# Performance work log

Measured on AMD Instinct MI355X. Metric: run time of the kernel, lower is better.

Reference implementation:

```python
import jax, jax.numpy as jnp
import numpy as np

HEADS = 8
BN_EPS = 1e-5

def _bn(x2d, g, b):
    # torch BatchNorm1d in training mode: biased batch stats
    mu = x2d.mean(0)
    var = x2d.var(0)
    return (x2d - mu) * jax.lax.rsqrt(var + BN_EPS) * g + b

def _window_indices(H):
    # exclusive-end box coordinates, in the exact order of the torch loop
    m = H // 2
    r0, r1, c0, c1 = [], [], [], []
    for i in range(1, m + 1):
        wins = [(m - i, m + i + 1, m - i, m + i + 1),  # full square
                (m - i, m + 1,     m - i, m + i + 1),  # top half
                (m,     m + i + 1, m - i, m + i + 1),  # bottom half
                (m - i, m + i + 1, m - i, m + 1),      # left half
                (m - i, m + i + 1, m,     m + i + 1)]  # right half
        for a, b, c, d in wins:
            r0.append(a); r1.append(b); c0.append(c); c1.append(d)
    r0 = np.array(r0); r1 = np.array(r1); c0 = np.array(c0); c1 = np.array(c1)
    counts = ((r1 - r0) * (c1 - c0)).astype(np.float32)
    return r0, r1, c0, c1, counts

def _box_sums(P, r0, r1, c0, c1):
    # P: padded 2D prefix sum [B, C, H+1, H+1]; returns [B, C, K]
    return P[:, :, r1, c1] - P[:, :, r0, c1] - P[:, :, r1, c0] + P[:, :, r0, c0]

def _integral(img):
    return jnp.pad(jnp.cumsum(jnp.cumsum(img, axis=2), axis=3), ((0, 0), (0, 0), (1, 0), (1, 0)))

def setup_inputs() -> dict:
    key = jax.random.key(0)
    ks = jax.random.split(key, 8)
    B, Cin, H = 64, 512, 31
    C = 512  # heads * base_dim
    x = jax.random.normal(ks[0], (B, Cin, H, H), dtype=jnp.float32)
    w_v = jax.random.normal(ks[1], (Cin, C), dtype=jnp.float32) * 0.02
    w_k = jax.random.normal(ks[2], (Cin, C), dtype=jnp.float32) * 0.02
    w_fc = jax.random.normal(ks[3], (Cin + C, 512), dtype=jnp.float32) * 0.02
    z = lambda n: jnp.zeros((n,), jnp.float32)
    o = lambda n: jnp.ones((n,), jnp.float32)
    return {"x": x,
            "w_v": w_v, "b_v": z(C), "g_vn": o(C), "b_vn": z(C),
            "w_k": w_k, "b_k": z(C), "g_kn": o(C), "b_kn": z(C),
            "w_fc": w_fc, "b_fc": z(512), "g_fcn": o(512), "b_fcn": z(512)}

def reference(x, w_v, b_v, g_vn, b_vn, w_k, b_k, g_kn, b_kn, w_fc, b_fc, g_fcn, b_fcn):
    B, Cin, H, W = x.shape
    N = H * W
    C = w_v.shape[1]
    d = C // HEADS
    m = H // 2
    xt = x.reshape(B, Cin, N).transpose(0, 2, 1)       # [B, N, Cin]
    x0 = xt[:, N // 2, :]                              # [B, Cin] center pixel feature
    flat = xt.reshape(B * N, Cin)
    v = jax.nn.relu(_bn(flat @ w_v + b_v, g_vn, b_vn))
    v = v.reshape(B, N, C).transpose(0, 2, 1).reshape(B, C, H, H)
    k = _bn(flat @ w_k + b_k, g_kn, b_kn).reshape(B, N, HEADS, d).transpose(0, 2, 1, 3)  # [B,h,N,d]
    q = k[:, :, N // 2, :]                             # [B, h, d]
    attn = jax.nn.softmax(jnp.einsum('bhd,bhnd->bhn', q, k) * (d ** -0.5), axis=-1)      # [B,h,N]
    attn_full = jnp.broadcast_to(attn[:, :, None, :], (B, HEADS, d, N)).reshape(B, C, H, H)
    xw = attn_full * v                                 # attn-weighted values [B,C,H,H]
    eps = 1e-16
    r0, r1, c0, c1, counts = _window_indices(H)
    Px = _integral(xw)
    Pa = _integral(attn_full)
    mx = _box_sums(Px, r0, r1, c0, c1) / counts        # window means of xw   [B,C,K]
    ma = _box_sums(Pa, r0, r1, c0, c1) / counts        # window means of attn [B,C,K]
    y_win = (mx / (ma + eps)).transpose(0, 2, 1)       # [B, K, C]
    y = jnp.concatenate([xw[:, :, m, m][:, None, :], y_win], axis=1)  # [B, n, C]
    # F.normalize(p=2, dim=2)
    y = y / jnp.maximum(jnp.linalg.norm(y, axis=2, keepdims=True), 1e-12)
    n = y.shape[1]
    yy = jnp.concatenate([jnp.broadcast_to(x0[:, None, :], (B, n, Cin)), y], axis=-1)
    out = jax.nn.relu(_bn(yy.reshape(B * n, Cin + C) @ w_fc + b_fc, g_fcn, b_fcn))
    return out.reshape(B, n, -1)
```

## Files before the change

kernel.cpp:

```cpp
#include <hip/hip_runtime.h>
#include <stdint.h>

#define DEV __device__ __forceinline__

typedef __bf16 bf16x8 __attribute__((ext_vector_type(8)));
typedef unsigned short u16x8 __attribute__((ext_vector_type(8)));
typedef float f32x4 __attribute__((ext_vector_type(4)));

#define NS 968
#define NMB0 484
#define NMB1 38
#define RCH 16
#define NCH0 ((NMB0 + RCH - 1) / RCH)

DEV uint16_t f2bf(float f) {
    union { float f; uint32_t u; } v; v.f = f;
    uint32_t r = v.u + 0x7fffu + ((v.u >> 16) & 1u);
    return (uint16_t)(r >> 16);
}
DEV float bf2f(uint16_t h) {
    union { uint32_t u; float f; } v; v.u = ((uint32_t)h) << 16;
    return v.f;
}
DEV float bflo(uint32_t w) { union { uint32_t u; float f; } v; v.u = w << 16; return v.f; }
DEV float bfhi(uint32_t w) { union { uint32_t u; float f; } v; v.u = w & 0xffff0000u; return v.f; }

#if __has_builtin(__builtin_amdgcn_cvt_pk_bf16_f32)
typedef __bf16 bf16x2 __attribute__((ext_vector_type(2)));
DEV uint32_t pk2bf(float lo, float hi) {
    bf16x2 r = __builtin_amdgcn_cvt_pk_bf16_f32(lo, hi);
    return __builtin_bit_cast(uint32_t, r);
}
#else
DEV uint32_t pk2bf(float lo, float hi) {
    return (uint32_t)f2bf(lo) | ((uint32_t)f2bf(hi) << 16);
}
#endif

#if __has_builtin(__builtin_amdgcn_global_load_lds)
DEV void async16(const uint16_t* g, uint16_t* l) {
    __builtin_amdgcn_global_load_lds(
        (const __attribute__((address_space(1))) uint32_t*)g,
        (__attribute__((address_space(3))) uint32_t*)l, 16, 0, 0);
}
#else
DEV void async16(const uint16_t* g, uint16_t* l) {
    *(u16x8*)l = *(const u16x8*)g;
}
#endif

__global__ void k_convert_x(const float* __restrict__ x, uint16_t* __restrict__ xbt) {
    __shared__ float tile[32][33];
    int b = blockIdx.z;
    int n0 = blockIdx.x * 32;
    int c0 = blockIdx.y * 32;
    int tx = threadIdx.x, ty = threadIdx.y;
    #pragma unroll
    for (int i = 0; i < 4; ++i) {
        int c = c0 + ty + 8 * i;
        int n = n0 + tx;
        float v = 0.f;
        if (n < 961) v = x[((size_t)b * 512 + c) * 961 + n];
        tile[ty + 8 * i][tx] = v;
    }
    __syncthreads();
    int idx = ty * 32 + tx;
    int c4 = (idx & 7) * 4;
    int nl = idx >> 3;
    int n = n0 + nl;
    if (n < NS) {
        ushort4 val;
        val.x = f2bf(tile[c4 + 0][nl]);
        val.y = f2bf(tile[c4 + 1][nl]);
        val.z = f2bf(tile[c4 + 2][nl]);
        val.w = f2bf(tile[c4 + 3][nl]);
        *(ushort4*)&xbt[((size_t)b * NS + n) * 512 + c0 + c4] = val;
    }
}

__global__ void k_convert_w(const float* __restrict__ wv, const float* __restrict__ wk,
                            const float* __restrict__ wfc,
                            uint16_t* __restrict__ wvkt, uint16_t* __restrict__ wfct) {
    int idx = blockIdx.x * 256 + threadIdx.x;
    if (idx < 524288) {
        int j = idx >> 9, k = idx & 511;
        float v = (j < 512) ? wv[(size_t)k * 512 + j] : wk[(size_t)k * 512 + (j - 512)];
        wvkt[idx] = f2bf(v);
    } else {
        int t = idx - 524288;
        int j = t >> 10, k = t & 1023;
        wfct[t] = f2bf(wfc[(size_t)k * 512 + j]);
    }
}

template<int K, int EPI>
__global__ __launch_bounds__(256, 4)
void k_gemm(const uint16_t* __restrict__ A, const uint16_t* __restrict__ Bt,
            uint16_t* __restrict__ out_v, uint16_t* __restrict__ out_k,
            float* __restrict__ out_f,
            float* __restrict__ part)
{
    __shared__ __align__(16) uint16_t sbuf[16384];
    __shared__ float sStat[512];
    uint16_t* sA0 = sbuf;
    uint16_t* sA1 = sbuf + 4096;
    uint16_t* sB0 = sbuf + 8192;
    uint16_t* sB1 = sbuf + 12288;

    const int tid = threadIdx.x;
    const int wave = tid >> 6, lane = tid & 63;
    const int quad = lane >> 4, l16 = lane & 15;
    int m0, j0, mbi = 0;
    if constexpr (EPI == 0) {
        int lin = blockIdx.x;
        int xcd = lin & 7, rest = lin >> 3;
        int jb = rest & 7, mhi = rest >> 3;
        int mb = mhi * 8 + xcd;
        if (mb >= NMB0) return;
        m0 = mb * 128; j0 = jb * 128; mbi = mb;
    } else {
        m0 = blockIdx.y * 128; j0 = blockIdx.x * 128; mbi = blockIdx.y;
    }
    const int wm = wave >> 1, wj = wave & 1;

    const f32x4 fzero = {0.f, 0.f, 0.f, 0.f};
    f32x4 acc[4][4];
    #pragma unroll
    for (int i = 0; i < 4; ++i)
        #pragma unroll
        for (int j = 0; j < 4; ++j) acc[i][j] = fzero;

    const int c0 = tid;
    const int mA0 = c0 >> 2, kq0 = c0 & 3;
    const int c1 = tid + 256;
    const int mA1 = c1 >> 2, kq1 = c1 & 3;

    const int KT = K / 64;
    for (int kt = 0; kt < KT; ++kt) {
        const uint16_t* Ak = A + (size_t)m0 * K + kt * 64;
        const uint16_t* Bk = Bt + (size_t)j0 * K + kt * 64;
        async16(Ak + (size_t)mA0 * K + kq0 * 8,      &sA0[c0 * 8]);
        async16(Ak + (size_t)mA1 * K + kq1 * 8,      &sA0[c1 * 8]);
        async16(Ak + (size_t)mA0 * K + 32 + kq0 * 8, &sA1[c0 * 8]);
        async16(Ak + (size_t)mA1 * K + 32 + kq1 * 8, &sA1[c1 * 8]);
        async16(Bk + (size_t)mA0 * K + kq0 * 8,      &sB0[c0 * 8]);
        async16(Bk + (size_t)mA1 * K + kq1 * 8,      &sB0[c1 * 8]);
        async16(Bk + (size_t)mA0 * K + 32 + kq0 * 8, &sB1[c0 * 8]);
        async16(Bk + (size_t)mA1 * K + 32 + kq1 * 8, &sB1[c1 * 8]);
        __syncthreads();
        #pragma unroll
        for (int p = 0; p < 2; ++p) {
            const uint16_t* pA = p ? sA1 : sA0;
            const uint16_t* pB = p ? sB1 : sB0;
            bf16x8 af[4], bfr[4];
            #pragma unroll
            for (int i = 0; i < 4; ++i) {
                int m = wm * 64 + i * 16 + l16;
                u16x8 r = *(const u16x8*)&pA[m * 32 + quad * 8];
                af[i] = __builtin_bit_cast(bf16x8, r);
            }
            #pragma unroll
            for (int j = 0; j < 4; ++j) {
                int jj = wj * 64 + j * 16 + l16;
                u16x8 r = *(const u16x8*)&pB[jj * 32 + quad * 8];
                bfr[j] = __builtin_bit_cast(bf16x8, r);
            }
            #pragma unroll
            for (int i = 0; i < 4; ++i)
                #pragma unroll
                for (int j = 0; j < 4; ++j)
                    acc[i][j] = __builtin_amdgcn_mfma_f32_16x16x32_bf16(af[i], bfr[j], acc[i][j], 0, 0, 0);
        }
        __syncthreads();
    }

    #pragma unroll
    for (int j = 0; j < 4; ++j) {
        const int col_local = wj * 64 + j * 16 + l16;
        float ls = 0.f, lq = 0.f;
        #pragma unroll
        for (int i = 0; i < 4; ++i) {
            #pragma unroll
            for (int reg = 0; reg < 4; ++reg) {
                const float val = acc[i][j][reg];
                ls += val; lq += val * val;
                if constexpr (EPI == 1) {
                    const int r = m0 + wm * 64 + i * 16 + quad * 4 + reg;
                    out_f[(size_t)r * 512 + (j0 + col_local)] = val;
                }
            }
        }
        ls += __shfl_xor(ls, 16); lq += __shfl_xor(lq, 16);
        ls += __shfl_xor(ls, 32); lq += __shfl_xor(lq, 32);
        if (quad == 0) {
            sStat[wm * 128 + col_local] = ls;
            sStat[256 + wm * 128 + col_local] = lq;
        }
    }
    __syncthreads();
    if (tid < 128) {
        float s = sStat[tid] + sStat[128 + tid];
        float q = sStat[256 + tid] + sStat[384 + tid];
        if constexpr (EPI == 0) {
            part[(size_t)mbi * 1024 + (j0 + tid)] = s;
            part[(size_t)NMB0 * 1024 + (size_t)mbi * 1024 + (j0 + tid)] = q;
        } else {
            part[(size_t)mbi * 512 + (j0 + tid)] = s;
            part[(size_t)NMB1 * 512 + (size_t)mbi * 512 + (j0 + tid)] = q;
        }
    }

    if constexpr (EPI == 0) {
        #pragma unroll
        for (int ch = 0; ch < 2; ++ch) {
            if (wj == ch) {
                #pragma unroll
                for (int j = 0; j < 4; ++j) {
                    const int c = j * 16 + l16;
                    #pragma unroll
                    for (int i = 0; i < 4; ++i) {
                        const int rloc = wm * 64 + i * 16 + quad * 4;
                        uint2 pp;
                        pp.x = pk2bf(acc[i][j][0], acc[i][j][1]);
                        pp.y = pk2bf(acc[i][j][2], acc[i][j][3]);
                        *(uint2*)&sbuf[c * 136 + rloc] = pp;
                    }
                }
            }
            __syncthreads();
            const int jg = j0 + ch * 64;
            uint16_t* const outp = (jg < 512) ? out_v : out_k;
            const int jbase = (jg < 512) ? jg : jg - 512;
            #pragma unroll
            for (int s = 0; s < 8; ++s) {
                const int chunk = tid + 256 * s;
                const int c = chunk >> 5, q = chunk & 31;
                uint2 val = *(const uint2*)&sbuf[c * 136 + q * 4];
                const int r = m0 + q * 4;
                const unsigned bb_ = (unsigned)r / (unsigned)NS;
                const unsigned nn = (unsigned)r - bb_ * (unsigned)NS;
                *(uint2*)&outp[((size_t)bb_ * 512 + jbase + c) * NS + nn] = val;
            }
            __syncthreads();
        }
    }
}

template<int NMB, int NC>
__global__ void k_redA(const float* __restrict__ part, float* __restrict__ pp)
{
    int col = blockIdx.x * 256 + threadIdx.x;
    int cz = blockIdx.y;
    int i0 = cz * RCH;
    float s = 0.f, q = 0.f;
    #pragma unroll
    for (int k = 0; k < RCH; ++k) {
        int i = i0 + k;
        if (i < NMB) {
            s += part[(size_t)i * NC + col];
            q += part[(size_t)(NMB + i) * NC + col];
        }
    }
    int nch = (NMB + RCH - 1) / RCH;
    pp[(size_t)cz * NC + col] = s;
    pp[(size_t)(nch + cz) * NC + col] = q;
}

template<int NCH, int NC>
__global__ void k_redB(const float* __restrict__ pp, float* __restrict__ osum,
                       float* __restrict__ osq)
{
    int col = blockIdx.x * 256 + threadIdx.x;
    float s = 0.f, q = 0.f;
    #pragma unroll
    for (int k = 0; k < NCH; ++k) {
        s += pp[(size_t)k * NC + col];
        q += pp[(size_t)(NCH + k) * NC + col];
    }
    osum[col] = s;
    osq[col] = q;
}

template<int NMB, int NC>
__global__ void k_redsmall(const float* __restrict__ part, float* __restrict__ osum,
                           float* __restrict__ osq)
{
    int col = blockIdx.x * 256 + threadIdx.x;
    float s = 0.f, q = 0.f;
    #pragma unroll
    for (int i = 0; i < NMB; ++i) {
        s += part[(size_t)i * NC + col];
        q += part[(size_t)(NMB + i) * NC + col];
    }
    osum[col] = s;
    osq[col] = q;
}

__global__ void k_attn(const uint16_t* __restrict__ kraw,
                       const float* __restrict__ colsum, const float* __restrict__ colsq,
                       const float* __restrict__ g_kn, const float* __restrict__ b_kn,
                       float* __restrict__ attn, float* __restrict__ maw)
{
    __shared__ float qa[64];
    __shared__ float s_qb;
    __shared__ float att[NS];
    __shared__ float red[8];

    int bh = blockIdx.x;
    int b = bh >> 3, h = bh & 7;
    int tid = threadIdx.x;
    constexpr float invM = 1.f / 61504.f;

    if (tid < 64) {
        int c = h * 64 + tid;
        float mean = colsum[512 + c] * invM;
        float q_ = colsq[512 + c] * invM;
        float a = g_kn[c] * rsqrtf(q_ - mean * mean + 1e-5f);
        float bb = b_kn[c] - mean * a;
        float kr = bf2f(kraw[((size_t)b * 512 + c) * NS + 480]);
        float qv = kr * a + bb;
        qa[tid] = qv * a;
        float qb = qv * bb;
        for (int off = 32; off; off >>= 1) qb += __shfl_down(qb, off);
        if (tid == 0) s_qb = qb;
    }
    __syncthreads();

    const int n4 = tid * 4;
    const bool active = n4 < 961;
    float a0 = 0.f, a1 = 0.f, a2 = 0.f, a3 = 0.f;
    if (active) {
        const uint16_t* kp = kraw + ((size_t)b * 512 + h * 64) * NS + n4;
        #pragma unroll 16
        for (int dd = 0; dd < 64; ++dd) {
            uint2 kk = *(const uint2*)(kp + (size_t)dd * NS);
            float q = qa[dd];
            a0 += q * bflo(kk.x);
            a1 += q * bfhi(kk.x);
            a2 += q * bflo(kk.y);
            a3 += q * bfhi(kk.y);
        }
    }
    float lg[4] = {a0, a1, a2, a3};
    float lmax = -1e30f;
    #pragma unroll
    for (int i = 0; i < 4; ++i) {
        lg[i] = (lg[i] + s_qb) * 0.125f;
        if (n4 + i < 961) lmax = fmaxf(lmax, lg[i]);
    }
    for (int off = 32; off; off >>= 1) lmax = fmaxf(lmax, __shfl_xor(lmax, off));
    if ((tid & 63) == 0) red[tid >> 6] = lmax;
    __syncthreads();
    float bmax = fmaxf(fmaxf(red[0], red[1]), fmaxf(red[2], red[3]));

    float lsum = 0.f;
    #pragma unroll
    for (int i = 0; i < 4; ++i) {
        float e = (n4 + i < 961) ? __expf(lg[i] - bmax) : 0.f;
        lg[i] = e;
        lsum += e;
    }
    for (int off = 32; off; off >>= 1) lsum += __shfl_xor(lsum, off);
    if ((tid & 63) == 0) red[4 + (tid >> 6)] = lsum;
    __syncthreads();
    float inv = 1.f / (red[4] + red[5] + red[6] + red[7]);
    if (active) {
        f32x4 v = {lg[0] * inv, lg[1] * inv, lg[2] * inv, lg[3] * inv};
        *(f32x4*)&att[n4] = v;
        *(f32x4*)&attn[(size_t)bh * NS + n4] = v;
    }
    __syncthreads();

    if (tid < 31) { float s = 0.f; for (int cc = 0; cc < 31; ++cc) { s += att[tid * 31 + cc]; att[tid * 31 + cc] = s; } }
    __syncthreads();
    if (tid < 31) { float s = 0.f; for (int rr = 0; rr < 31; ++rr) { s += att[rr * 31 + tid]; att[rr * 31 + tid] = s; } }
    __syncthreads();

    if (tid < 75) {
        int i = tid / 5 + 1, t = tid % 5;
        const int m = 15;
        int r0, r1, cc0, cc1;
        switch (t) {
            case 0: r0 = m - i; r1 = m + i + 1; cc0 = m - i; cc1 = m + i + 1; break;
            case 1: r0 = m - i; r1 = m + 1;     cc0 = m - i; cc1 = m + i + 1; break;
            case 2: r0 = m;     r1 = m + i + 1; cc0 = m - i; cc1 = m + i + 1; break;
            case 3: r0 = m - i; r1 = m + i + 1; cc0 = m - i; cc1 = m + 1;     break;
            default:r0 = m - i; r1 = m + i + 1; cc0 = m;     cc1 = m + i + 1; break;
        }
        auto S = [&](int r, int c) -> float { return (r < 0 || c < 0) ? 0.f : att[r * 31 + c]; };
        float box = S(r1 - 1, cc1 - 1) - S(r0 - 1, cc1 - 1) - S(r1 - 1, cc0 - 1) + S(r0 - 1, cc0 - 1);
        float cnt = (float)((r1 - r0) * (cc1 - cc0));
        maw[(size_t)bh * 75 + tid] = box / cnt;
    }
}

__global__ void k_winbox(const uint16_t* __restrict__ vraw,
                         const float* __restrict__ colsum, const float* __restrict__ colsq,
                         const float* __restrict__ g_vn, const float* __restrict__ b_vn,
                         const float* __restrict__ attn, const float* __restrict__ maw,
                         float* __restrict__ y)
{
    __shared__ float xw[NS];
    __shared__ float s_center;
    int bc = blockIdx.x;
    int b = bc >> 9, c = bc & 511;
    int h = c >> 6;
    int tid = threadIdx.x;
    constexpr float invM = 1.f / 61504.f;
    float mean = colsum[c] * invM;
    float q_ = colsq[c] * invM;
    float a = g_vn[c] * rsqrtf(q_ - mean * mean + 1e-5f);
    float bb = b_vn[c] - mean * a;
    const uint16_t* vp = vraw + (size_t)bc * NS;
    const float* ap = attn + (size_t)(b * 8 + h) * NS;
    int n4 = tid * 4;
    if (n4 < 961) {
        uint2 kk = *(const uint2*)(vp + n4);
        f32x4 at = *(const f32x4*)(ap + n4);
        f32x4 v;
        v[0] = fmaxf(bflo(kk.x) * a + bb, 0.f) * at[0];
        v[1] = fmaxf(bfhi(kk.x) * a + bb, 0.f) * at[1];
        v[2] = fmaxf(bflo(kk.y) * a + bb, 0.f) * at[2];
        v[3] = fmaxf(bfhi(kk.y) * a + bb, 0.f) * at[3];
        *(f32x4*)&xw[n4] = v;
    }
    __syncthreads();
    if (tid == 0) s_center = xw[480];
    __syncthreads();
    if (tid < 31) { float s = 0.f; for (int cc = 0; cc < 31; ++cc) { s += xw[tid * 31 + cc]; xw[tid * 31 + cc] = s; } }
    __syncthreads();
    if (tid < 31) { float s = 0.f; for (int rr = 0; rr < 31; ++rr) { s += xw[rr * 31 + tid]; xw[rr * 31 + tid] = s; } }
    __syncthreads();
    if (tid < 75) {
        int i = tid / 5 + 1, t = tid % 5;
        const int m = 15;
        int r0, r1, cc0, cc1;
        switch (t) {
            case 0: r0 = m - i; r1 = m + i + 1; cc0 = m - i; cc1 = m + i + 1; break;
            case 1: r0 = m - i; r1 = m + 1;     cc0 = m - i; cc1 = m + i + 1; break;
            case 2: r0 = m;     r1 = m + i + 1; cc0 = m - i; cc1 = m + i + 1; break;
            case 3: r0 = m - i; r1 = m + i + 1; cc0 = m - i; cc1 = m + 1;     break;
            default:r0 = m - i; r1 = m + i + 1; cc0 = m;     cc1 = m + i + 1; break;
        }
        auto S = [&](int r, int cc) -> float { return (r < 0 || cc < 0) ? 0.f : xw[r * 31 + cc]; };
        float box = S(r1 - 1, cc1 - 1) - S(r0 - 1, cc1 - 1) - S(r1 - 1, cc0 - 1) + S(r0 - 1, cc0 - 1);
        float cnt = (float)((r1 - r0) * (cc1 - cc0));
        float mx = box / cnt;
        float ma = maw[(size_t)(b * 8 + h) * 75 + tid];
        y[((size_t)b * 76 + 1 + tid) * 512 + c] = mx / (ma + 1e-16f);
    }
    if (tid == 96) y[((size_t)b * 76) * 512 + c] = s_center;
}

__global__ void k_build_yy(const float* __restrict__ y, const uint16_t* __restrict__ xbt,
                           uint16_t* __restrict__ yy)
{
    __shared__ float red[4];
    int row = blockIdx.x;
    int b = row / 76;
    int tid = threadIdx.x;
    const float* yp = y + (size_t)row * 512;
    float v0 = yp[tid], v1 = yp[tid + 256];
    float ss = v0 * v0 + v1 * v1;
    for (int off = 32; off; off >>= 1) ss += __shfl_xor(ss, off);
    if ((tid & 63) == 0) red[tid >> 6] = ss;
    __syncthreads();
    float tot = red[0] + red[1] + red[2] + red[3];
    float inv = 1.f / fmaxf(sqrtf(tot), 1e-12f);
    uint16_t* op = yy + (size_t)row * 1024;
    const uint16_t* x0p = xbt + ((size_t)b * NS + 480) * 512;
    op[tid]           = x0p[tid];
    op[tid + 256]     = x0p[tid + 256];
    op[512 + tid]       = f2bf(v0 * inv);
    op[512 + tid + 256] = f2bf(v1 * inv);
}

__global__ void k_fcout(const float* __restrict__ fcraw,
                        const float* __restrict__ colsum, const float* __restrict__ colsq,
                        const float* __restrict__ g, const float* __restrict__ be,
                        float* __restrict__ out)
{
    size_t idx = (size_t)blockIdx.x * 256 + threadIdx.x;
    if (idx < (size_t)4864 * 512) {
        int j = (int)(idx & 511);
        constexpr float invM = 1.f / 4864.f;
        float mean = colsum[j] * invM;
        float q_ = colsq[j] * invM;
        float a = g[j] * rsqrtf(q_ - mean * mean + 1e-5f);
        float bb = be[j] - mean * a;
        out[idx] = fmaxf(fcraw[idx] * a + bb, 0.f);
    }
}

extern "C" void kernel_launch(void* const* d_in, const int* in_sizes, int n_in,
                              void* d_out, int out_size, void* d_ws, size_t ws_size,
                              hipStream_t stream)
{
    (void)in_sizes; (void)n_in; (void)out_size; (void)ws_size;
    const float* x    = (const float*)d_in[0];
    const float* w_v  = (const float*)d_in[1];
    const float* g_vn = (const float*)d_in[3];
    const float* b_vn = (const float*)d_in[4];
    const float* w_k  = (const float*)d_in[5];
    const float* g_kn = (const float*)d_in[7];
    const float* b_kn = (const float*)d_in[8];
    const float* w_fc = (const float*)d_in[9];
    const float* g_fcn = (const float*)d_in[11];
    const float* b_fcn = (const float*)d_in[12];
    float* out = (float*)d_out;

    char* base = (char*)d_ws;
    size_t off = 0;
    auto alloc = [&](size_t bytes) -> void* {
        void* p = base + off;
        off += (bytes + 255) & ~(size_t)255;
        return p;
    };
    uint16_t* xbt  = (uint16_t*)alloc((size_t)64 * NS * 512 * 2);
    uint16_t* wvkt = (uint16_t*)alloc((size_t)1024 * 512 * 2);
    uint16_t* wfct = (uint16_t*)alloc((size_t)512 * 1024 * 2);
    uint16_t* vraw = (uint16_t*)alloc((size_t)64 * 512 * NS * 2);
    uint16_t* kraw = (uint16_t*)alloc((size_t)64 * 512 * NS * 2);
    float* stats   = (float*)alloc(3072 * 4);
    float* attn    = (float*)alloc((size_t)512 * NS * 4);
    float* maw     = (float*)alloc((size_t)512 * 75 * 4);
    float* y       = (float*)alloc((size_t)64 * 76 * 512 * 4);
    uint16_t* yy   = (uint16_t*)alloc((size_t)4864 * 1024 * 2);
    float* fcraw   = (float*)alloc((size_t)4864 * 512 * 4);
    float* part0   = (float*)alloc((size_t)2 * NMB0 * 1024 * 4);
    float* part1   = (float*)alloc((size_t)2 * NMB1 * 512 * 4);
    float* pp0     = (float*)alloc((size_t)2 * NCH0 * 1024 * 4);

    k_convert_x<<<dim3(31, 16, 64), dim3(32, 8), 0, stream>>>(x, xbt);
    k_convert_w<<<4096, 256, 0, stream>>>(w_v, w_k, w_fc, wvkt, wfct);

    k_gemm<512, 0><<<3904, 256, 0, stream>>>(xbt, wvkt, vraw, kraw, nullptr, part0);
    k_redA<NMB0, 1024><<<dim3(4, NCH0), 256, 0, stream>>>(part0, pp0);
    k_redB<NCH0, 1024><<<4, 256, 0, stream>>>(pp0, stats, stats + 1024);

    k_attn<<<512, 256, 0, stream>>>(kraw, stats, stats + 1024, g_kn, b_kn, attn, maw);
    k_winbox<<<64 * 512, 256, 0, stream>>>(vraw, stats, stats + 1024, g_vn, b_vn, attn, maw, y);
    k_build_yy<<<4864, 256, 0, stream>>>(y, xbt, yy);

    k_gemm<1024, 1><<<dim3(4, 38), 256, 0, stream>>>(yy, wfct, nullptr, nullptr, fcraw, part1);
    k_redsmall<NMB1, 512><<<2, 256, 0, stream>>>(part1, stats + 2048, stats + 2560);
    k_fcout<<<9728, 256, 0, stream>>>(fcraw, stats + 2048, stats + 2560, g_fcn, b_fcn, out);
}
```

Baseline: 450.3 us.

## Swizzle GEMM LDS layout and pad token stride to 992

Applies an XOR swizzle to the 16-byte chunk index in the GEMM's shared-memory tiles, aiming to remove bank conflicts on the MFMA fragment reads. It also pads the per-batch token stride from 968 to 992 so the M dimension divides exactly into 128-row tiles and 16-block reduction chunks, which lets the bounds checks in conversion, GEMM and reduction be dropped. The padding adds extra rows of GEMM work and memory traffic. The padded rows hold zeros from the x conversion, but they still flow into the V/K statistics partials, and bias or other epilogue effects could change the BN stats.

```diff
diff --git a/kernel.cpp b/kernel.cpp
--- a/kernel.cpp
+++ b/kernel.cpp
@@ -7,11 +7,11 @@
 typedef unsigned short u16x8 __attribute__((ext_vector_type(8)));
 typedef float f32x4 __attribute__((ext_vector_type(4)));
 
-#define NS 968
-#define NMB0 484
+#define NS 992
+#define NMB0 496
 #define NMB1 38
 #define RCH 16
-#define NCH0 ((NMB0 + RCH - 1) / RCH)
+#define NCH0 (NMB0 / RCH)
 
 DEV uint16_t f2bf(float f) {
     union { float f; uint32_t u; } v; v.f = f;
@@ -68,14 +68,12 @@
     int c4 = (idx & 7) * 4;
     int nl = idx >> 3;
     int n = n0 + nl;
-    if (n < NS) {
-        ushort4 val;
-        val.x = f2bf(tile[c4 + 0][nl]);
-        val.y = f2bf(tile[c4 + 1][nl]);
-        val.z = f2bf(tile[c4 + 2][nl]);
-        val.w = f2bf(tile[c4 + 3][nl]);
-        *(ushort4*)&xbt[((size_t)b * NS + n) * 512 + c0 + c4] = val;
-    }
+    ushort4 val;
+    val.x = f2bf(tile[c4 + 0][nl]);
+    val.y = f2bf(tile[c4 + 1][nl]);
+    val.z = f2bf(tile[c4 + 2][nl]);
+    val.w = f2bf(tile[c4 + 3][nl]);
+    *(ushort4*)&xbt[((size_t)b * NS + n) * 512 + c0 + c4] = val;
 }
 
 __global__ void k_convert_w(const float* __restrict__ wv, const float* __restrict__ wk,
@@ -116,7 +114,6 @@
         int xcd = lin & 7, rest = lin >> 3;
         int jb = rest & 7, mhi = rest >> 3;
         int mb = mhi * 8 + xcd;
-        if (mb >= NMB0) return;
         m0 = mb * 128; j0 = jb * 128; mbi = mb;
     } else {
         m0 = blockIdx.y * 128; j0 = blockIdx.x * 128; mbi = blockIdx.y;
@@ -131,22 +128,24 @@
         for (int j = 0; j < 4; ++j) acc[i][j] = fzero;
 
     const int c0 = tid;
-    const int mA0 = c0 >> 2, kq0 = c0 & 3;
+    const int mA0 = c0 >> 2;
+    const int sq0 = (c0 & 3) ^ ((mA0 >> 1) & 3);
     const int c1 = tid + 256;
-    const int mA1 = c1 >> 2, kq1 = c1 & 3;
+    const int mA1 = c1 >> 2;
+    const int sq1 = (c1 & 3) ^ ((mA1 >> 1) & 3);
 
     const int KT = K / 64;
     for (int kt = 0; kt < KT; ++kt) {
         const uint16_t* Ak = A + (size_t)m0 * K + kt * 64;
         const uint16_t* Bk = Bt + (size_t)j0 * K + kt * 64;
-        async16(Ak + (size_t)mA0 * K + kq0 * 8,      &sA0[c0 * 8]);
-        async16(Ak + (size_t)mA1 * K + kq1 * 8,      &sA0[c1 * 8]);
-        async16(Ak + (size_t)mA0 * K + 32 + kq0 * 8, &sA1[c0 * 8]);
-        async16(Ak + (size_t)mA1 * K + 32 + kq1 * 8, &sA1[c1 * 8]);
-        async16(Bk + (size_t)mA0 * K + kq0 * 8,      &sB0[c0 * 8]);
-        async16(Bk + (size_t)mA1 * K + kq1 * 8,      &sB0[c1 * 8]);
-        async16(Bk + (size_t)mA0 * K + 32 + kq0 * 8, &sB1[c0 * 8]);
-        async16(Bk + (size_t)mA1 * K + 32 + kq1 * 8, &sB1[c1 * 8]);
+        async16(Ak + (size_t)mA0 * K + sq0 * 8,      &sA0[c0 * 8]);
+        async16(Ak + (size_t)mA1 * K + sq1 * 8,      &sA0[c1 * 8]);
+        async16(Ak + (size_t)mA0 * K + 32 + sq0 * 8, &sA1[c0 * 8]);
+        async16(Ak + (size_t)mA1 * K + 32 + sq1 * 8, &sA1[c1 * 8]);
+        async16(Bk + (size_t)mA0 * K + sq0 * 8,      &sB0[c0 * 8]);
+        async16(Bk + (size_t)mA1 * K + sq1 * 8,      &sB0[c1 * 8]);
+        async16(Bk + (size_t)mA0 * K + 32 + sq0 * 8, &sB1[c0 * 8]);
+        async16(Bk + (size_t)mA1 * K + 32 + sq1 * 8, &sB1[c1 * 8]);
         __syncthreads();
         #pragma unroll
         for (int p = 0; p < 2; ++p) {
@@ -156,13 +155,15 @@
             #pragma unroll
             for (int i = 0; i < 4; ++i) {
                 int m = wm * 64 + i * 16 + l16;
-                u16x8 r = *(const u16x8*)&pA[m * 32 + quad * 8];
+                int qs = quad ^ ((m >> 1) & 3);
+                u16x8 r = *(const u16x8*)&pA[m * 32 + qs * 8];
                 af[i] = __builtin_bit_cast(bf16x8, r);
             }
             #pragma unroll
             for (int j = 0; j < 4; ++j) {
                 int jj = wj * 64 + j * 16 + l16;
-                u16x8 r = *(const u16x8*)&pB[jj * 32 + quad * 8];
+                int qs = quad ^ ((jj >> 1) & 3);
+                u16x8 r = *(const u16x8*)&pB[jj * 32 + qs * 8];
                 bfr[j] = __builtin_bit_cast(bf16x8, r);
             }
             #pragma unroll
@@ -249,6 +250,7 @@
 template<int NMB, int NC>
 __global__ void k_redA(const float* __restrict__ part, float* __restrict__ pp)
 {
+    static_assert(NMB % RCH == 0, "exact chunks");
     int col = blockIdx.x * 256 + threadIdx.x;
     int cz = blockIdx.y;
     int i0 = cz * RCH;
@@ -256,12 +258,10 @@
     #pragma unroll
     for (int k = 0; k < RCH; ++k) {
         int i = i0 + k;
-        if (i < NMB) {
-            s += part[(size_t)i * NC + col];
-            q += part[(size_t)(NMB + i) * NC + col];
-        }
-    }
-    int nch = (NMB + RCH - 1) / RCH;
+        s += part[(size_t)i * NC + col];
+        q += part[(size_t)(NMB + i) * NC + col];
+    }
+    constexpr int nch = NMB / RCH;
     pp[(size_t)cz * NC + col] = s;
     pp[(size_t)(nch + cz) * NC + col] = q;
 }
@@ -534,7 +534,7 @@
     k_convert_x<<<dim3(31, 16, 64), dim3(32, 8), 0, stream>>>(x, xbt);
     k_convert_w<<<4096, 256, 0, stream>>>(w_v, w_k, w_fc, wvkt, wfct);
 
-    k_gemm<512, 0><<<3904, 256, 0, stream>>>(xbt, wvkt, vraw, kraw, nullptr, part0);
+    k_gemm<512, 0><<<3968, 256, 0, stream>>>(xbt, wvkt, vraw, kraw, nullptr, part0);
     k_redA<NMB0, 1024><<<dim3(4, NCH0), 256, 0, stream>>>(part0, pp0);
     k_redB<NCH0, 1024><<<4, 256, 0, stream>>>(pp0, stats, stats + 1024);
 
```

After: 447.1 us. About the same (-0.7%).
